# Kernel tuning notes

Measured on AMD Instinct MI355X. Metric: run time of the kernel, lower is better.

## Reference

```python
import jax, jax.numpy as jnp
import numpy as np

B, N, D, H, P, S = 2, 40962, 128, 4, 100, 512
HD = D // H  # 32
EPS = 1e-5


def setup_inputs() -> dict:
    key = jax.random.key(0)
    ks = jax.random.split(key, 8)
    s = 1.0 / np.sqrt(D)
    x = jax.random.normal(ks[0], (B, N, D), jnp.float32)
    Wq = jax.random.normal(ks[1], (D, D), jnp.float32) * s
    Wk = jax.random.normal(ks[2], (D, D), jnp.float32) * s
    Wv = jax.random.normal(ks[3], (D, D), jnp.float32) * s
    Wo = jax.random.normal(ks[4], (D, D), jnp.float32) * s
    bq = jnp.zeros((D,), jnp.float32)
    bk = jnp.zeros((D,), jnp.float32)
    bv = jnp.zeros((D,), jnp.float32)
    bo = jnp.zeros((D,), jnp.float32)
    ln_g = jnp.ones((D,), jnp.float32)
    ln_b = jnp.zeros((D,), jnp.float32)
    patch_indices = jax.random.randint(ks[5], (P, S), 0, N)  # node ids per patch slot
    core_mask = jax.random.uniform(ks[6], (P, S)) < 0.8       # core vs overlap slots
    return dict(x=x, Wq=Wq, bq=bq, Wk=Wk, bk=bk, Wv=Wv, bv=bv, Wo=Wo, bo=bo,
                ln_g=ln_g, ln_b=ln_b, patch_indices=patch_indices, core_mask=core_mask)


def reference(x, Wq, bq, Wk, bk, Wv, bv, Wo, bo, ln_g, ln_b, patch_indices, core_mask):
    # gather: [B, P, S, D]
    px = x[:, patch_indices]

    def proj(W, b):
        return (px @ W.T + b).reshape(B, P, S, H, HD)

    q = proj(Wq, bq)
    k = proj(Wk, bk)
    v = proj(Wv, bv)

    # per-patch multi-head attention
    scores = jnp.einsum('bpshd,bpthd->bphst', q, k) / np.sqrt(HD).astype(np.float32)
    attn = jax.nn.softmax(scores, axis=-1)  # dropout is identity in eval
    att = jnp.einsum('bphst,bpthd->bpshd', attn, v).reshape(B, P, S, D)
    patch_out = att @ Wo.T + bo  # [B, P, S, D]

    # scatter-add only core slots back to nodes, with overlap-count normalization
    cm = core_mask.astype(x.dtype)
    patch_out = patch_out * cm[None, :, :, None]
    idx = patch_indices.reshape(-1)  # [P*S]
    vals = patch_out.reshape(B, P * S, D).transpose(1, 0, 2)  # [P*S, B, D]
    agg = jax.ops.segment_sum(vals, idx, num_segments=N).transpose(1, 0, 2)  # [B, N, D]
    cnt = jax.ops.segment_sum(cm.reshape(-1), idx, num_segments=N)  # [N]
    out = agg / jnp.clip(cnt, 1.0)[None, :, None]

    # residual + LayerNorm
    h = x + out
    mu = jnp.mean(h, axis=-1, keepdims=True)
    var = jnp.mean((h - mu) ** 2, axis=-1, keepdims=True)
    return (h - mu) / jnp.sqrt(var + EPS) * ln_g + ln_b
```

## Files before the change

kernel.cpp:

```cpp
#include <hip/hip_runtime.h>
#include <hip/hip_bf16.h>
#include <hip/hip_fp16.h>

#define B_ 2
#define N_ 40962
#define D_ 128
#define H_ 4
#define P_ 100
#define S_ 512
#define T_ 102400
#define PS_ 51200
#define CAP_ 32

typedef unsigned short u16;
typedef unsigned int u32;
typedef _Float16 f16x4 __attribute__((ext_vector_type(4)));
typedef _Float16 f16x8 __attribute__((ext_vector_type(8)));
typedef float f32x4 __attribute__((ext_vector_type(4)));

#define OFF_Q    0ull
#define OFF_K    26214400ull
#define OFF_V    52428800ull
#define OFF_BP   78643200ull
#define OFF_CNT  78774272ull
#define OFF_CM   78938120ull
#define OFF_FLAG 79142920ull
#define CUR_BYTES ((size_t)N_ * 4)

__device__ __forceinline__ u32 pack2h(float a, float b) {
  __half2 h = __floats2half2_rn(a, b);
  return __builtin_bit_cast(u32, h);
}
__device__ __forceinline__ f16x8 cat8(uint2 lo, uint2 hi) {
  return __builtin_bit_cast(f16x8, make_uint4(lo.x, lo.y, hi.x, hi.y));
}

__device__ __forceinline__ f32x4 mfma32(f16x8 a, f16x8 b, f32x4 c) {
#if __has_builtin(__builtin_amdgcn_mfma_f32_16x16x32_f16)
  return __builtin_amdgcn_mfma_f32_16x16x32_f16(a, b, c, 0, 0, 0);
#else
  f16x4 alo = {a[0], a[1], a[2], a[3]}, ahi = {a[4], a[5], a[6], a[7]};
  f16x4 blo = {b[0], b[1], b[2], b[3]}, bhi = {b[4], b[5], b[6], b[7]};
  c = __builtin_amdgcn_mfma_f32_16x16x16f16(alo, blo, c, 0, 0, 0);
  return __builtin_amdgcn_mfma_f32_16x16x16f16(ahi, bhi, c, 0, 0, 0);
#endif
}

__device__ __forceinline__ bool mask_on(const void* mask, int fl, int i) {
  if (fl & 1) return ((const unsigned char*)mask)[i] != 0;
  if (fl & 2) return ((const float*)mask)[i] != 0.f;
  return ((const int*)mask)[i] != 0;
}

__global__ void probe_mask_k(const unsigned char* __restrict__ mb, int* __restrict__ flag) {
  int i = blockIdx.x * 256 + threadIdx.x;
  int f = 0;
  unsigned char v = mb[i];
  if (v) {
    int m4 = i & 3;
    if (m4 == 1) f |= 1;
    else if (m4 == 3) f |= 2;
  }
#pragma unroll
  for (int m = 32; m >= 1; m >>= 1) f |= __shfl_xor(f, m);
  if ((threadIdx.x & 63) == 0 && f) atomicOr(flag, f);
}

__global__ void mask_cnt_k(const void* __restrict__ mask, const int* __restrict__ pidx,
                           const int* __restrict__ flag, float* __restrict__ cm,
                           float* __restrict__ cnt) {
  int i = blockIdx.x * 256 + threadIdx.x;
  int fl = *flag;
  bool on = mask_on(mask, fl, i);
  cm[i] = on ? 1.f : 0.f;
  if (on) atomicAdd(&cnt[pidx[i]], 1.f);
}

__global__ void fill_k(const void* __restrict__ mask, const int* __restrict__ pidx,
                       const int* __restrict__ flag, int* __restrict__ cursor,
                       int* __restrict__ slots) {
  int i = blockIdx.x * 256 + threadIdx.x;
  int fl = *flag;
  if (mask_on(mask, fl, i)) {
    int n = pidx[i];
    int pos = atomicAdd(&cursor[n], 1);
    if (pos < CAP_) slots[n * CAP_ + pos] = i;
  }
}

__global__ void pack_w_k(const float* __restrict__ Wq, const float* __restrict__ Wk,
                         const float* __restrict__ Wv, const float* __restrict__ Wo,
                         u16* __restrict__ bp) {
  int gi = blockIdx.x * 256 + threadIdx.x;
  int m = gi >> 12;
  int r = gi & 4095;
  int fi = r >> 6;
  int l = r & 63;
  int nt = fi >> 3, ks = fi & 7;
  const float* W = (m == 0) ? Wq : (m == 1) ? Wk : (m == 2) ? Wv : Wo;
  int n = nt * 16 + (l & 15);
  int k0 = ks * 16 + ((l >> 4) << 2);
  float4 w = *(const float4*)(W + n * 128 + k0);
  *(uint2*)(bp + (size_t)gi * 4) = make_uint2(pack2h(w.x, w.y), pack2h(w.z, w.w));
}

__global__ __launch_bounds__(256) void qkv_k(
    const float* __restrict__ x, const int* __restrict__ pidx,
    const u16* __restrict__ bp,
    const float* __restrict__ bq, const float* __restrict__ bk, const float* __restrict__ bv,
    u16* __restrict__ qkv) {
  __shared__ uint4 As[64 * 16];
  int tid = threadIdx.x;
  int t0 = blockIdx.x * 64;
  {
    int r = tid >> 2, qd = tid & 3;
    int T = t0 + r;
    int b = T / PS_;
    int ps = T - b * PS_;
    int pi = pidx[ps];
    const float4* src = (const float4*)(x + ((size_t)b * N_ + pi) * D_ + qd * 32);
    u32 us[16];
#pragma unroll
    for (int j = 0; j < 8; j++) {
      float4 f = src[j];
      us[2 * j]     = pack2h(f.x, f.y);
      us[2 * j + 1] = pack2h(f.z, f.w);
    }
#pragma unroll
    for (int c = 0; c < 4; c++) {
      int byteoff = (qd * 64 + c * 16) ^ ((r & 7) << 4);
      As[r * 16 + (byteoff >> 4)] = make_uint4(us[4 * c], us[4 * c + 1], us[4 * c + 2], us[4 * c + 3]);
    }
  }
  __syncthreads();
  int lane = tid & 63, wid = tid >> 6;
  int l15 = lane & 15, l4 = lane >> 4;
  int wm = wid & 1, wn = wid >> 1;
  uint2 afr[2][8];
#pragma unroll
  for (int mt = 0; mt < 2; mt++) {
    int row = wm * 32 + mt * 16 + l15;
#pragma unroll
    for (int ks = 0; ks < 8; ks++) {
      int byteoff = (ks * 32 + (l4 << 3)) ^ ((row & 7) << 4);
      afr[mt][ks] = *(const uint2*)((const char*)As + row * 256 + byteoff);
    }
  }
  const uint2* bpp = (const uint2*)bp;
#pragma unroll 1
  for (int mat = 0; mat < 3; mat++) {
    uint2 bfrag[4][8];
#pragma unroll
    for (int nt = 0; nt < 4; nt++) {
      int ntg = wn * 4 + nt;
#pragma unroll
      for (int ks = 0; ks < 8; ks++)
        bfrag[nt][ks] = bpp[(mat * 64 + ntg * 8 + ks) * 64 + lane];
    }
    const float* bias = (mat == 0) ? bq : (mat == 1) ? bk : bv;
    f32x4 acc[2][4];
#pragma unroll
    for (int nt = 0; nt < 4; nt++) {
      float bvv = bias[wn * 64 + nt * 16 + l15];
#pragma unroll
      for (int mt = 0; mt < 2; mt++) {
        f32x4 z = {bvv, bvv, bvv, bvv};
        acc[mt][nt] = z;
      }
    }
#pragma unroll
    for (int kp = 0; kp < 4; kp++) {
#pragma unroll
      for (int mt = 0; mt < 2; mt++) {
        f16x8 a = cat8(afr[mt][2 * kp], afr[mt][2 * kp + 1]);
#pragma unroll
        for (int nt = 0; nt < 4; nt++) {
          f16x8 b = cat8(bfrag[nt][2 * kp], bfrag[nt][2 * kp + 1]);
          acc[mt][nt] = mfma32(a, b, acc[mt][nt]);
        }
      }
    }
    if (mat == 2) {
      u16* vt = qkv + (size_t)2 * T_ * D_;
#pragma unroll
      for (int mt = 0; mt < 2; mt++) {
        int rbase = t0 + wm * 32 + mt * 16 + (l4 << 2);
        int bpi = rbase >> 9;
        int s = rbase & 511;
#pragma unroll
        for (int nt = 0; nt < 4; nt++) {
          int col = wn * 64 + nt * 16 + l15;
          uint2 pv = make_uint2(pack2h(acc[mt][nt][0], acc[mt][nt][1]),
                                pack2h(acc[mt][nt][2], acc[mt][nt][3]));
          *(uint2*)(vt + ((size_t)(bpi * 4 + (col >> 5)) * 32 + (col & 31)) * 512 + s) = pv;
        }
      }
    } else if (mat == 1) {
      u16* kh = qkv + (size_t)T_ * D_;
#pragma unroll
      for (int mt = 0; mt < 2; mt++) {
        int rbase = t0 + wm * 32 + mt * 16 + (l4 << 2);
        int bpi = rbase >> 9;
        int s = rbase & 511;
#pragma unroll
        for (int nt = 0; nt < 4; nt++) {
          int col = wn * 64 + nt * 16 + l15;
          int hd = col & 31, ch = col >> 5;
#pragma unroll
          for (int i = 0; i < 4; i++) {
            __half hv = __float2half(acc[mt][nt][i]);
            kh[((size_t)(bpi * 4 + ch) * 512 + (s + i)) * 32 + hd] = __builtin_bit_cast(u16, hv);
          }
        }
      }
    } else {
      u16* outp = qkv;
#pragma unroll
      for (int mt = 0; mt < 2; mt++) {
        int rbase = t0 + wm * 32 + mt * 16 + (l4 << 2);
#pragma unroll
        for (int nt = 0; nt < 4; nt++) {
          int col = wn * 64 + nt * 16 + l15;
#pragma unroll
          for (int i = 0; i < 4; i++) {
            __half hv = __float2half(acc[mt][nt][i]);
            outp[(size_t)(rbase + i) * D_ + col] = __builtin_bit_cast(u16, hv);
          }
        }
      }
    }
  }
}

__global__ __launch_bounds__(512, 4) void attn_k(
    u16* wq_att, const u16* __restrict__ wk, const u16* __restrict__ wvt) {
  __shared__ __align__(16) u16 Ks[512 * 32];
  __shared__ __align__(16) u16 Vs[32 * 512];
  int tid = threadIdx.x;
  int bid = blockIdx.x;
  int h = bid & 3;
  int bp = bid >> 2;
  int lane = tid & 63, w = tid >> 6;
  int l15 = lane & 15, l4 = lane >> 4;
  size_t tbase = (size_t)bp * 512;
  int q0 = w * 64;
  {
    const u16* kg = wk + (size_t)(bp * 4 + h) * 512 * 32;
    const u16* vg = wvt + (size_t)(bp * 4 + h) * 32 * 512;
#pragma unroll
    for (int j = 0; j < 4; j++) {
      int i = j * 512 + tid;
      uint4 ku = *(const uint4*)(kg + (size_t)i * 8);
      int row = i >> 2, c = i & 3;
      int swk = (row >> 1) & 7;
      *(uint2*)(Ks + row * 32 + (((2 * c)     ^ swk) << 2)) = make_uint2(ku.x, ku.y);
      *(uint2*)(Ks + row * 32 + (((2 * c + 1) ^ swk) << 2)) = make_uint2(ku.z, ku.w);
      uint4 vu = *(const uint4*)(vg + (size_t)i * 8);
      int vr2 = i >> 6, vc = i & 63;
      int swv = vr2 & 15;
      *(uint2*)(Vs + vr2 * 512 + (((2 * vc)     ^ swv) << 2)) = make_uint2(vu.x, vu.y);
      *(uint2*)(Vs + vr2 * 512 + (((2 * vc + 1) ^ swv) << 2)) = make_uint2(vu.z, vu.w);
    }
  }
  uint4 qf8[4];
  {
    const u16* qbase = wq_att + (tbase + q0) * 128 + h * 32;
    const __half2 sc2 = __floats2half2_rn(0.25500527f, 0.25500527f);
#pragma unroll
    for (int nt = 0; nt < 4; nt++) {
      const u16* qr = qbase + (size_t)(nt * 16 + l15) * 128 + l4 * 4;
      uint2 u0 = *(const uint2*)(qr);
      uint2 u1 = *(const uint2*)(qr + 16);
      u32 w0 = __builtin_bit_cast(u32, __hmul2(__builtin_bit_cast(__half2, u0.x), sc2));
      u32 w1 = __builtin_bit_cast(u32, __hmul2(__builtin_bit_cast(__half2, u0.y), sc2));
      u32 w2 = __builtin_bit_cast(u32, __hmul2(__builtin_bit_cast(__half2, u1.x), sc2));
      u32 w3 = __builtin_bit_cast(u32, __hmul2(__builtin_bit_cast(__half2, u1.y), sc2));
      qf8[nt] = make_uint4(w0, w1, w2, w3);
    }
  }
  f32x4 O[2][4];
  f32x4 LS[4];
#pragma unroll
  for (int a = 0; a < 4; a++) {
    O[0][a] = (f32x4){0.f, 0.f, 0.f, 0.f};
    O[1][a] = (f32x4){0.f, 0.f, 0.f, 0.f};
    LS[a] = (f32x4){0.f, 0.f, 0.f, 0.f};
  }
  const f16x8 ones8 = {(_Float16)1.f, (_Float16)1.f, (_Float16)1.f, (_Float16)1.f,
                       (_Float16)1.f, (_Float16)1.f, (_Float16)1.f, (_Float16)1.f};
  __syncthreads();

  for (int t0 = 0; t0 < 512; t0 += 64) {
#pragma unroll
    for (int mp = 0; mp < 2; mp++) {
      int krA = t0 + mp * 32 + l15;
      int krB = krA + 16;
      const u16* kpA = Ks + krA * 32;
      const u16* kpB = Ks + krB * 32;
      int swkA = (krA >> 1) & 7;
      int swkB = (krB >> 1) & 7;
      uint2 a0A = *(const uint2*)(kpA + ((l4       ^ swkA) << 2));
      uint2 a1A = *(const uint2*)(kpA + (((4 + l4) ^ swkA) << 2));
      uint2 a0B = *(const uint2*)(kpB + ((l4       ^ swkB) << 2));
      uint2 a1B = *(const uint2*)(kpB + (((4 + l4) ^ swkB) << 2));
      f16x8 a8A = cat8(a0A, a1A);
      f16x8 a8B = cat8(a0B, a1B);
      int gA = (t0 >> 2) + mp * 8 + l4;
      int gB = gA + 4;
      uint2 vA0 = *(const uint2*)(Vs + l15 * 512        + ((gA ^ l15) << 2));
      uint2 vB0 = *(const uint2*)(Vs + l15 * 512        + ((gB ^ l15) << 2));
      uint2 vA1 = *(const uint2*)(Vs + (16 + l15) * 512 + ((gA ^ l15) << 2));
      uint2 vB1 = *(const uint2*)(Vs + (16 + l15) * 512 + ((gB ^ l15) << 2));
      f16x8 v80 = cat8(vA0, vB0);
      f16x8 v81 = cat8(vA1, vB1);
      __builtin_amdgcn_s_setprio(1);
#pragma unroll
      for (int nt = 0; nt < 4; nt++) {
        f16x8 qb = __builtin_bit_cast(f16x8, qf8[nt]);
        f32x4 z = {0.f, 0.f, 0.f, 0.f};
        f32x4 sA = mfma32(a8A, qb, z);
        f32x4 sB = mfma32(a8B, qb, z);
        float e0 = __builtin_amdgcn_exp2f(sA[0]);
        float e1 = __builtin_amdgcn_exp2f(sA[1]);
        float e2 = __builtin_amdgcn_exp2f(sA[2]);
        float e3 = __builtin_amdgcn_exp2f(sA[3]);
        float e4 = __builtin_amdgcn_exp2f(sB[0]);
        float e5 = __builtin_amdgcn_exp2f(sB[1]);
        float e6 = __builtin_amdgcn_exp2f(sB[2]);
        float e7 = __builtin_amdgcn_exp2f(sB[3]);
        uint4 pu = make_uint4(
            __builtin_bit_cast(u32, __builtin_amdgcn_cvt_pkrtz(e0, e1)),
            __builtin_bit_cast(u32, __builtin_amdgcn_cvt_pkrtz(e2, e3)),
            __builtin_bit_cast(u32, __builtin_amdgcn_cvt_pkrtz(e4, e5)),
            __builtin_bit_cast(u32, __builtin_amdgcn_cvt_pkrtz(e6, e7)));
        f16x8 pb = __builtin_bit_cast(f16x8, pu);
        LS[nt]   = mfma32(ones8, pb, LS[nt]);
        O[0][nt] = mfma32(v80, pb, O[0][nt]);
        O[1][nt] = mfma32(v81, pb, O[1][nt]);
      }
      __builtin_amdgcn_s_setprio(0);
    }
  }
#pragma unroll
  for (int nt = 0; nt < 4; nt++) {
    float r = 1.f / LS[nt][0];
#pragma unroll
    for (int mt2 = 0; mt2 < 2; mt2++) {
      uint2 ov = make_uint2(pack2h(O[mt2][nt][0] * r, O[mt2][nt][1] * r),
                            pack2h(O[mt2][nt][2] * r, O[mt2][nt][3] * r));
      *(uint2*)(wq_att + (tbase + q0 + nt * 16 + l15) * 128 + h * 32 + mt2 * 16 + l4 * 4) = ov;
    }
  }
}

__global__ __launch_bounds__(256) void proj_k(
    const u16* __restrict__ watt, const u16* __restrict__ bp, const float* __restrict__ bo,
    u16* __restrict__ po) {
  __shared__ uint4 As[64 * 16];
  int tid = threadIdx.x;
  int t0 = blockIdx.x * 64;
  {
    int r = tid >> 2, qd = tid & 3;
    const uint4* src = (const uint4*)(watt + (size_t)(t0 + r) * D_ + qd * 32);
#pragma unroll
    for (int c = 0; c < 4; c++) {
      int byteoff = (qd * 64 + c * 16) ^ ((r & 7) << 4);
      As[r * 16 + (byteoff >> 4)] = src[c];
    }
  }
  __syncthreads();
  int lane = tid & 63, wid = tid >> 6;
  int l15 = lane & 15, l4 = lane >> 4;
  int wm = wid & 1, wn = wid >> 1;
  uint2 bfrag[4][8];
  const uint2* bpp = (const uint2*)bp;
#pragma unroll
  for (int nt = 0; nt < 4; nt++) {
    int ntg = wn * 4 + nt;
#pragma unroll
    for (int ks = 0; ks < 8; ks++)
      bfrag[nt][ks] = bpp[(3 * 64 + ntg * 8 + ks) * 64 + lane];
  }
  uint2 afr[2][8];
#pragma unroll
  for (int tt = 0; tt < 2; tt++) {
    int row = wm * 32 + tt * 16 + l15;
#pragma unroll
    for (int ks = 0; ks < 8; ks++) {
      int byteoff = (ks * 32 + (l4 << 3)) ^ ((row & 7) << 4);
      afr[tt][ks] = *(const uint2*)((const char*)As + row * 256 + byteoff);
    }
  }
  f32x4 acc[4][2];
#pragma unroll
  for (int nt = 0; nt < 4; nt++) {
    float4 bo4 = *(const float4*)(bo + wn * 64 + nt * 16 + l4 * 4);
    f32x4 bz = {bo4.x, bo4.y, bo4.z, bo4.w};
    acc[nt][0] = bz;
    acc[nt][1] = bz;
  }
#pragma unroll
  for (int kp = 0; kp < 4; kp++) {
#pragma unroll
    for (int nt = 0; nt < 4; nt++) {
      f16x8 a = cat8(bfrag[nt][2 * kp], bfrag[nt][2 * kp + 1]);
#pragma unroll
      for (int tt = 0; tt < 2; tt++) {
        f16x8 b = cat8(afr[tt][2 * kp], afr[tt][2 * kp + 1]);
        acc[nt][tt] = mfma32(a, b, acc[nt][tt]);
      }
    }
  }
#pragma unroll
  for (int tt = 0; tt < 2; tt++) {
    size_t tok = t0 + wm * 32 + tt * 16 + l15;
#pragma unroll
    for (int nt = 0; nt < 4; nt++) {
      int n0 = wn * 64 + nt * 16 + l4 * 4;
      f32x4 a = acc[nt][tt];
      uint2 pv = make_uint2(pack2h(a[0], a[1]), pack2h(a[2], a[3]));
      *(uint2*)(po + tok * D_ + n0) = pv;
    }
  }
}

__global__ __launch_bounds__(256) void ln_k(
    const float* __restrict__ x, const float* __restrict__ cnt,
    const u16* __restrict__ po, const int* __restrict__ slots,
    const float* __restrict__ g, const float* __restrict__ bta, float* __restrict__ out) {
  int tid = threadIdx.x;
  int row = blockIdx.x * 8 + (tid >> 5);
  if (row >= B_ * N_) return;
  int l32 = tid & 31;
  int n = row % N_;
  int b = row / N_;
  float c = cnt[n];
  int deg = (int)c;
  if (deg > CAP_) deg = CAP_;
  float rc = 1.f / (c > 1.f ? c : 1.f);
  float4 a = make_float4(0.f, 0.f, 0.f, 0.f);
  const int* sl = slots + n * CAP_;
  for (int j = 0; j < deg; j++) {
    int s = sl[j];
    uint2 u = *(const uint2*)(po + ((size_t)b * PS_ + s) * D_ + l32 * 4);
    float2 a01 = __half22float2(__builtin_bit_cast(__half2, u.x));
    float2 a23 = __half22float2(__builtin_bit_cast(__half2, u.y));
    a.x += a01.x; a.y += a01.y; a.z += a23.x; a.w += a23.y;
  }
  size_t off = (size_t)row * D_ + l32 * 4;
  float4 xa = *(const float4*)(x + off);
  float4 hv = make_float4(fmaf(a.x, rc, xa.x), fmaf(a.y, rc, xa.y),
                          fmaf(a.z, rc, xa.z), fmaf(a.w, rc, xa.w));
  float s = hv.x + hv.y + hv.z + hv.w;
  float s2 = hv.x * hv.x + hv.y * hv.y + hv.z * hv.z + hv.w * hv.w;
#pragma unroll
  for (int m = 16; m >= 1; m >>= 1) {
    s += __shfl_xor(s, m);
    s2 += __shfl_xor(s2, m);
  }
  float mu = s * 0.0078125f;
  float var = s2 * 0.0078125f - mu * mu;
  float rstd = rsqrtf(var + 1e-5f);
  float4 gv = *(const float4*)(g + l32 * 4);
  float4 bv = *(const float4*)(bta + l32 * 4);
  float4 ov = make_float4((hv.x - mu) * rstd * gv.x + bv.x,
                          (hv.y - mu) * rstd * gv.y + bv.y,
                          (hv.z - mu) * rstd * gv.z + bv.z,
                          (hv.w - mu) * rstd * gv.w + bv.w);
  *(float4*)(out + off) = ov;
}

extern "C" void kernel_launch(void* const* d_in, const int* in_sizes, int n_in,
                              void* d_out, int out_size, void* d_ws, size_t ws_size,
                              hipStream_t stream) {
  const float* x   = (const float*)d_in[0];
  const float* Wq  = (const float*)d_in[1];
  const float* bq  = (const float*)d_in[2];
  const float* Wk  = (const float*)d_in[3];
  const float* bk  = (const float*)d_in[4];
  const float* Wv  = (const float*)d_in[5];
  const float* bv  = (const float*)d_in[6];
  const float* Wo  = (const float*)d_in[7];
  const float* bo  = (const float*)d_in[8];
  const float* lng = (const float*)d_in[9];
  const float* lnb = (const float*)d_in[10];
  const int* pidx  = (const int*)d_in[11];
  const void* cmask = d_in[12];
  float* out = (float*)d_out;
  char* ws = (char*)d_ws;

  u16* wsq = (u16*)(ws + OFF_Q);
  u16* wsk = (u16*)(ws + OFF_K);
  u16* wsvt = (u16*)(ws + OFF_V);
  u16* wbp = (u16*)(ws + OFF_BP);
  float* wcnt = (float*)(ws + OFF_CNT);
  float* wcm  = (float*)(ws + OFF_CM);
  int* wflag  = (int*)(ws + OFF_FLAG);
  u16* po = (u16*)(ws + OFF_K);
  int* cursor = (int*)(ws + OFF_V);
  int* slots = (int*)(ws + OFF_V + CUR_BYTES);

  hipMemsetAsync(ws + OFF_CNT, 0, (OFF_FLAG + 4) - OFF_CNT, stream);

  probe_mask_k<<<200, 256, 0, stream>>>((const unsigned char*)cmask, wflag);
  mask_cnt_k<<<200, 256, 0, stream>>>(cmask, pidx, wflag, wcm, wcnt);
  pack_w_k<<<64, 256, 0, stream>>>(Wq, Wk, Wv, Wo, wbp);
  qkv_k<<<1600, 256, 0, stream>>>(x, pidx, wbp, bq, bk, bv, wsq);
  attn_k<<<800, 512, 0, stream>>>(wsq, wsk, wsvt);
  hipMemsetAsync(cursor, 0, CUR_BYTES, stream);
  fill_k<<<200, 256, 0, stream>>>(cmask, pidx, wflag, cursor, slots);
  proj_k<<<1600, 256, 0, stream>>>(wsq, wbp, bo, po);
  ln_k<<<10241, 256, 0, stream>>>(x, wcnt, po, slots, lng, lnb, out);
}
```

Before: 157.5 us.

## Drop LDS staging in QKV and attention K, load fragments directly from global

The QKV projection kernel now gathers x rows straight into MFMA A-fragments from global memory, removing the shared-memory staging and barrier. For Q and K it swaps operand roles so each lane writes contiguous 4-element vectors instead of scalar u16 stores. The attention kernel no longer stages K in LDS and reads K fragments directly from global (relying on cache), and its launch bounds occupancy hint is raised from 4 to 8. The trade is more uncoalesced global and cache traffic for K reads and gathered x rows, in exchange for less LDS use, fewer syncs and potentially higher occupancy.

```diff
diff --git a/kernel.cpp b/kernel.cpp
--- a/kernel.cpp
+++ b/kernel.cpp
@@ -109,44 +109,31 @@
     const u16* __restrict__ bp,
     const float* __restrict__ bq, const float* __restrict__ bk, const float* __restrict__ bv,
     u16* __restrict__ qkv) {
-  __shared__ uint4 As[64 * 16];
   int tid = threadIdx.x;
   int t0 = blockIdx.x * 64;
-  {
-    int r = tid >> 2, qd = tid & 3;
-    int T = t0 + r;
-    int b = T / PS_;
-    int ps = T - b * PS_;
-    int pi = pidx[ps];
-    const float4* src = (const float4*)(x + ((size_t)b * N_ + pi) * D_ + qd * 32);
-    u32 us[16];
-#pragma unroll
-    for (int j = 0; j < 8; j++) {
-      float4 f = src[j];
-      us[2 * j]     = pack2h(f.x, f.y);
-      us[2 * j + 1] = pack2h(f.z, f.w);
-    }
-#pragma unroll
-    for (int c = 0; c < 4; c++) {
-      int byteoff = (qd * 64 + c * 16) ^ ((r & 7) << 4);
-      As[r * 16 + (byteoff >> 4)] = make_uint4(us[4 * c], us[4 * c + 1], us[4 * c + 2], us[4 * c + 3]);
-    }
-  }
-  __syncthreads();
   int lane = tid & 63, wid = tid >> 6;
   int l15 = lane & 15, l4 = lane >> 4;
   int wm = wid & 1, wn = wid >> 1;
   uint2 afr[2][8];
 #pragma unroll
-  for (int mt = 0; mt < 2; mt++) {
-    int row = wm * 32 + mt * 16 + l15;
+  for (int tt = 0; tt < 2; tt++) {
+    int tok = t0 + wm * 32 + tt * 16 + l15;
+    int b = (tok >= PS_) ? 1 : 0;
+    int ps = tok - b * PS_;
+    int pi = pidx[ps];
+    const float* rp = x + ((size_t)b * N_ + pi) * D_;
 #pragma unroll
     for (int ks = 0; ks < 8; ks++) {
-      int byteoff = (ks * 32 + (l4 << 3)) ^ ((row & 7) << 4);
-      afr[mt][ks] = *(const uint2*)((const char*)As + row * 256 + byteoff);
+      float4 f = *(const float4*)(rp + ks * 16 + l4 * 4);
+      afr[tt][ks] = make_uint2(
+          __builtin_bit_cast(u32, __builtin_amdgcn_cvt_pkrtz(f.x, f.y)),
+          __builtin_bit_cast(u32, __builtin_amdgcn_cvt_pkrtz(f.z, f.w)));
     }
   }
   const uint2* bpp = (const uint2*)bp;
+  u16* qout = qkv;
+  u16* kh = qkv + (size_t)T_ * D_;
+  u16* vt = qkv + (size_t)2 * T_ * D_;
 #pragma unroll 1
   for (int mat = 0; mat < 3; mat++) {
     uint2 bfrag[4][8];
@@ -157,84 +144,87 @@
       for (int ks = 0; ks < 8; ks++)
         bfrag[nt][ks] = bpp[(mat * 64 + ntg * 8 + ks) * 64 + lane];
     }
-    const float* bias = (mat == 0) ? bq : (mat == 1) ? bk : bv;
-    f32x4 acc[2][4];
-#pragma unroll
-    for (int nt = 0; nt < 4; nt++) {
-      float bvv = bias[wn * 64 + nt * 16 + l15];
-#pragma unroll
-      for (int mt = 0; mt < 2; mt++) {
-        f32x4 z = {bvv, bvv, bvv, bvv};
-        acc[mt][nt] = z;
-      }
-    }
-#pragma unroll
-    for (int kp = 0; kp < 4; kp++) {
-#pragma unroll
-      for (int mt = 0; mt < 2; mt++) {
-        f16x8 a = cat8(afr[mt][2 * kp], afr[mt][2 * kp + 1]);
+    if (mat < 2) {
+      const float* bias = (mat == 0) ? bq : bk;
+      f32x4 acc[4][2];
+#pragma unroll
+      for (int nt = 0; nt < 4; nt++) {
+        float4 b4 = *(const float4*)(bias + wn * 64 + nt * 16 + l4 * 4);
+        f32x4 bz = {b4.x, b4.y, b4.z, b4.w};
+        acc[nt][0] = bz;
+        acc[nt][1] = bz;
+      }
+#pragma unroll
+      for (int kp = 0; kp < 4; kp++) {
 #pragma unroll
         for (int nt = 0; nt < 4; nt++) {
-          f16x8 b = cat8(bfrag[nt][2 * kp], bfrag[nt][2 * kp + 1]);
-          acc[mt][nt] = mfma32(a, b, acc[mt][nt]);
+          f16x8 a = cat8(bfrag[nt][2 * kp], bfrag[nt][2 * kp + 1]);
+#pragma unroll
+          for (int tt = 0; tt < 2; tt++) {
+            f16x8 b = cat8(afr[tt][2 * kp], afr[tt][2 * kp + 1]);
+            acc[nt][tt] = mfma32(a, b, acc[nt][tt]);
+          }
         }
       }
-    }
-    if (mat == 2) {
-      u16* vt = qkv + (size_t)2 * T_ * D_;
+#pragma unroll
+      for (int tt = 0; tt < 2; tt++) {
+        int tok = t0 + wm * 32 + tt * 16 + l15;
+#pragma unroll
+        for (int nt = 0; nt < 4; nt++) {
+          int n0 = wn * 64 + nt * 16 + l4 * 4;
+          f32x4 a = acc[nt][tt];
+          uint2 pv = make_uint2(pack2h(a[0], a[1]), pack2h(a[2], a[3]));
+          if (mat == 0) {
+            *(uint2*)(qout + (size_t)tok * D_ + n0) = pv;
+          } else {
+            int bpi = tok >> 9, s = tok & 511;
+            int ch = n0 >> 5, hd = n0 & 31;
+            *(uint2*)(kh + ((size_t)(bpi * 4 + ch) * 512 + s) * 32 + hd) = pv;
+          }
+        }
+      }
+    } else {
+      f32x4 acc[2][4];
+#pragma unroll
+      for (int nt = 0; nt < 4; nt++) {
+        float bvv = bv[wn * 64 + nt * 16 + l15];
+#pragma unroll
+        for (int mt = 0; mt < 2; mt++) {
+          f32x4 z = {bvv, bvv, bvv, bvv};
+          acc[mt][nt] = z;
+        }
+      }
+#pragma unroll
+      for (int kp = 0; kp < 4; kp++) {
+#pragma unroll
+        for (int mt = 0; mt < 2; mt++) {
+          f16x8 a = cat8(afr[mt][2 * kp], afr[mt][2 * kp + 1]);
+#pragma unroll
+          for (int nt = 0; nt < 4; nt++) {
+            f16x8 b = cat8(bfrag[nt][2 * kp], bfrag[nt][2 * kp + 1]);
+            acc[mt][nt] = mfma32(a, b, acc[mt][nt]);
+          }
+        }
+      }
 #pragma unroll
       for (int mt = 0; mt < 2; mt++) {
         int rbase = t0 + wm * 32 + mt * 16 + (l4 << 2);
         int bpi = rbase >> 9;
-        int s = rbase & 511;
+        int s0 = rbase & 511;
 #pragma unroll
         for (int nt = 0; nt < 4; nt++) {
           int col = wn * 64 + nt * 16 + l15;
           uint2 pv = make_uint2(pack2h(acc[mt][nt][0], acc[mt][nt][1]),
                                 pack2h(acc[mt][nt][2], acc[mt][nt][3]));
-          *(uint2*)(vt + ((size_t)(bpi * 4 + (col >> 5)) * 32 + (col & 31)) * 512 + s) = pv;
+          *(uint2*)(vt + ((size_t)(bpi * 4 + (col >> 5)) * 32 + (col & 31)) * 512 + s0) = pv;
         }
       }
-    } else if (mat == 1) {
-      u16* kh = qkv + (size_t)T_ * D_;
-#pragma unroll
-      for (int mt = 0; mt < 2; mt++) {
-        int rbase = t0 + wm * 32 + mt * 16 + (l4 << 2);
-        int bpi = rbase >> 9;
-        int s = rbase & 511;
-#pragma unroll
-        for (int nt = 0; nt < 4; nt++) {
-          int col = wn * 64 + nt * 16 + l15;
-          int hd = col & 31, ch = col >> 5;
-#pragma unroll
-          for (int i = 0; i < 4; i++) {
-            __half hv = __float2half(acc[mt][nt][i]);
-            kh[((size_t)(bpi * 4 + ch) * 512 + (s + i)) * 32 + hd] = __builtin_bit_cast(u16, hv);
-          }
-        }
-      }
-    } else {
-      u16* outp = qkv;
-#pragma unroll
-      for (int mt = 0; mt < 2; mt++) {
-        int rbase = t0 + wm * 32 + mt * 16 + (l4 << 2);
-#pragma unroll
-        for (int nt = 0; nt < 4; nt++) {
-          int col = wn * 64 + nt * 16 + l15;
-#pragma unroll
-          for (int i = 0; i < 4; i++) {
-            __half hv = __float2half(acc[mt][nt][i]);
-            outp[(size_t)(rbase + i) * D_ + col] = __builtin_bit_cast(u16, hv);
-          }
-        }
-      }
-    }
-  }
-}
-
-__global__ __launch_bounds__(512, 4) void attn_k(
+    }
+  }
+}
+
+__global__ __launch_bounds__(512, 8) void attn_k(
     u16* wq_att, const u16* __restrict__ wk, const u16* __restrict__ wvt) {
-  __shared__ __align__(16) u16 Ks[512 * 32];
   __shared__ __align__(16) u16 Vs[32 * 512];
   int tid = threadIdx.x;
   int bid = blockIdx.x;
@@ -244,17 +234,12 @@
   int l15 = lane & 15, l4 = lane >> 4;
   size_t tbase = (size_t)bp * 512;
   int q0 = w * 64;
+  const u16* kg = wk + (size_t)(bp * 4 + h) * 512 * 32;
   {
-    const u16* kg = wk + (size_t)(bp * 4 + h) * 512 * 32;
     const u16* vg = wvt + (size_t)(bp * 4 + h) * 32 * 512;
 #pragma unroll
     for (int j = 0; j < 4; j++) {
       int i = j * 512 + tid;
-      uint4 ku = *(const uint4*)(kg + (size_t)i * 8);
-      int row = i >> 2, c = i & 3;
-      int swk = (row >> 1) & 7;
-      *(uint2*)(Ks + row * 32 + (((2 * c)     ^ swk) << 2)) = make_uint2(ku.x, ku.y);
-      *(uint2*)(Ks + row * 32 + (((2 * c + 1) ^ swk) << 2)) = make_uint2(ku.z, ku.w);
       uint4 vu = *(const uint4*)(vg + (size_t)i * 8);
       int vr2 = i >> 6, vc = i & 63;
       int swv = vr2 & 15;
@@ -293,16 +278,12 @@
   for (int t0 = 0; t0 < 512; t0 += 64) {
 #pragma unroll
     for (int mp = 0; mp < 2; mp++) {
-      int krA = t0 + mp * 32 + l15;
-      int krB = krA + 16;
-      const u16* kpA = Ks + krA * 32;
-      const u16* kpB = Ks + krB * 32;
-      int swkA = (krA >> 1) & 7;
-      int swkB = (krB >> 1) & 7;
-      uint2 a0A = *(const uint2*)(kpA + ((l4       ^ swkA) << 2));
-      uint2 a1A = *(const uint2*)(kpA + (((4 + l4) ^ swkA) << 2));
-      uint2 a0B = *(const uint2*)(kpB + ((l4       ^ swkB) << 2));
-      uint2 a1B = *(const uint2*)(kpB + (((4 + l4) ^ swkB) << 2));
+      const u16* kpA = kg + (size_t)(t0 + mp * 32 + l15) * 32;
+      const u16* kpB = kpA + 16 * 32;
+      uint2 a0A = *(const uint2*)(kpA + l4 * 4);
+      uint2 a1A = *(const uint2*)(kpA + 16 + l4 * 4);
+      uint2 a0B = *(const uint2*)(kpB + l4 * 4);
+      uint2 a1B = *(const uint2*)(kpB + 16 + l4 * 4);
       f16x8 a8A = cat8(a0A, a1A);
       f16x8 a8B = cat8(a0B, a1B);
       int gA = (t0 >> 2) + mp * 8 + l4;
```

Result: slower. 525.3 us (+233.5%).

## Drop mask_cnt kernel, reuse fill cursor counts, read K directly from global

Applied to the files above, without the earlier changes.

Removes the mask_cnt_k kernel and its float atomics, taking the per-node core count from the cursor array that fill_k already builds, and shrinks the initial memset to the flag word. In attention, the K tile is no longer staged through swizzled shared memory; each wave loads its K fragments straight from global/L2. This cuts a launch, atomics and half the LDS footprint, which may raise occupancy, at the cost of repeated global K reads by all eight waves per block.

```diff
diff --git a/kernel.cpp b/kernel.cpp
--- a/kernel.cpp
+++ b/kernel.cpp
@@ -22,8 +22,6 @@
 #define OFF_K    26214400ull
 #define OFF_V    52428800ull
 #define OFF_BP   78643200ull
-#define OFF_CNT  78774272ull
-#define OFF_CM   78938120ull
 #define OFF_FLAG 79142920ull
 #define CUR_BYTES ((size_t)N_ * 4)
 
@@ -64,16 +62,6 @@
 #pragma unroll
   for (int m = 32; m >= 1; m >>= 1) f |= __shfl_xor(f, m);
   if ((threadIdx.x & 63) == 0 && f) atomicOr(flag, f);
-}
-
-__global__ void mask_cnt_k(const void* __restrict__ mask, const int* __restrict__ pidx,
-                           const int* __restrict__ flag, float* __restrict__ cm,
-                           float* __restrict__ cnt) {
-  int i = blockIdx.x * 256 + threadIdx.x;
-  int fl = *flag;
-  bool on = mask_on(mask, fl, i);
-  cm[i] = on ? 1.f : 0.f;
-  if (on) atomicAdd(&cnt[pidx[i]], 1.f);
 }
 
 __global__ void fill_k(const void* __restrict__ mask, const int* __restrict__ pidx,
@@ -234,7 +222,6 @@
 
 __global__ __launch_bounds__(512, 4) void attn_k(
     u16* wq_att, const u16* __restrict__ wk, const u16* __restrict__ wvt) {
-  __shared__ __align__(16) u16 Ks[512 * 32];
   __shared__ __align__(16) u16 Vs[32 * 512];
   int tid = threadIdx.x;
   int bid = blockIdx.x;
@@ -244,17 +231,12 @@
   int l15 = lane & 15, l4 = lane >> 4;
   size_t tbase = (size_t)bp * 512;
   int q0 = w * 64;
+  const u16* kg = wk + (size_t)(bp * 4 + h) * 512 * 32;
   {
-    const u16* kg = wk + (size_t)(bp * 4 + h) * 512 * 32;
     const u16* vg = wvt + (size_t)(bp * 4 + h) * 32 * 512;
 #pragma unroll
     for (int j = 0; j < 4; j++) {
       int i = j * 512 + tid;
-      uint4 ku = *(const uint4*)(kg + (size_t)i * 8);
-      int row = i >> 2, c = i & 3;
-      int swk = (row >> 1) & 7;
-      *(uint2*)(Ks + row * 32 + (((2 * c)     ^ swk) << 2)) = make_uint2(ku.x, ku.y);
-      *(uint2*)(Ks + row * 32 + (((2 * c + 1) ^ swk) << 2)) = make_uint2(ku.z, ku.w);
       uint4 vu = *(const uint4*)(vg + (size_t)i * 8);
       int vr2 = i >> 6, vc = i & 63;
       int swv = vr2 & 15;
@@ -293,16 +275,12 @@
   for (int t0 = 0; t0 < 512; t0 += 64) {
 #pragma unroll
     for (int mp = 0; mp < 2; mp++) {
-      int krA = t0 + mp * 32 + l15;
-      int krB = krA + 16;
-      const u16* kpA = Ks + krA * 32;
-      const u16* kpB = Ks + krB * 32;
-      int swkA = (krA >> 1) & 7;
-      int swkB = (krB >> 1) & 7;
-      uint2 a0A = *(const uint2*)(kpA + ((l4       ^ swkA) << 2));
-      uint2 a1A = *(const uint2*)(kpA + (((4 + l4) ^ swkA) << 2));
-      uint2 a0B = *(const uint2*)(kpB + ((l4       ^ swkB) << 2));
-      uint2 a1B = *(const uint2*)(kpB + (((4 + l4) ^ swkB) << 2));
+      const u16* kpA = kg + (size_t)(t0 + mp * 32 + l15) * 32;
+      const u16* kpB = kpA + 16 * 32;
+      uint2 a0A = *(const uint2*)(kpA + l4 * 4);
+      uint2 a1A = *(const uint2*)(kpA + 16 + l4 * 4);
+      uint2 a0B = *(const uint2*)(kpB + l4 * 4);
+      uint2 a1B = *(const uint2*)(kpB + 16 + l4 * 4);
       f16x8 a8A = cat8(a0A, a1A);
       f16x8 a8B = cat8(a0B, a1B);
       int gA = (t0 >> 2) + mp * 8 + l4;
@@ -425,7 +403,7 @@
 }
 
 __global__ __launch_bounds__(256) void ln_k(
-    const float* __restrict__ x, const float* __restrict__ cnt,
+    const float* __restrict__ x, const int* __restrict__ cursor,
     const u16* __restrict__ po, const int* __restrict__ slots,
     const float* __restrict__ g, const float* __restrict__ bta, float* __restrict__ out) {
   int tid = threadIdx.x;
@@ -434,10 +412,9 @@
   int l32 = tid & 31;
   int n = row % N_;
   int b = row / N_;
-  float c = cnt[n];
-  int deg = (int)c;
-  if (deg > CAP_) deg = CAP_;
-  float rc = 1.f / (c > 1.f ? c : 1.f);
+  int cnt = cursor[n];
+  int deg = cnt > CAP_ ? CAP_ : cnt;
+  float rc = 1.f / (float)(cnt > 1 ? cnt : 1);
   float4 a = make_float4(0.f, 0.f, 0.f, 0.f);
   const int* sl = slots + n * CAP_;
   for (int j = 0; j < deg; j++) {
@@ -493,22 +470,19 @@
   u16* wsk = (u16*)(ws + OFF_K);
   u16* wsvt = (u16*)(ws + OFF_V);
   u16* wbp = (u16*)(ws + OFF_BP);
-  float* wcnt = (float*)(ws + OFF_CNT);
-  float* wcm  = (float*)(ws + OFF_CM);
   int* wflag  = (int*)(ws + OFF_FLAG);
   u16* po = (u16*)(ws + OFF_K);
   int* cursor = (int*)(ws + OFF_V);
   int* slots = (int*)(ws + OFF_V + CUR_BYTES);
 
-  hipMemsetAsync(ws + OFF_CNT, 0, (OFF_FLAG + 4) - OFF_CNT, stream);
+  hipMemsetAsync(wflag, 0, 4, stream);
 
   probe_mask_k<<<200, 256, 0, stream>>>((const unsigned char*)cmask, wflag);
-  mask_cnt_k<<<200, 256, 0, stream>>>(cmask, pidx, wflag, wcm, wcnt);
   pack_w_k<<<64, 256, 0, stream>>>(Wq, Wk, Wv, Wo, wbp);
   qkv_k<<<1600, 256, 0, stream>>>(x, pidx, wbp, bq, bk, bv, wsq);
   attn_k<<<800, 512, 0, stream>>>(wsq, wsk, wsvt);
   hipMemsetAsync(cursor, 0, CUR_BYTES, stream);
   fill_k<<<200, 256, 0, stream>>>(cmask, pidx, wflag, cursor, slots);
   proj_k<<<1600, 256, 0, stream>>>(wsq, wbp, bo, po);
-  ln_k<<<10241, 256, 0, stream>>>(x, wcnt, po, slots, lng, lnb, out);
-}
+  ln_k<<<10241, 256, 0, stream>>>(x, cursor, po, slots, lng, lnb, out);
+}
```

Result: no change. 157.0 us (-0.3%).
